# Performance work log

Measured on AMD Instinct MI355X. Metric: run time of the kernel, lower is better.

The kernel has to match this reference:

```python
import jax, jax.numpy as jnp
import numpy as np
from jax import lax

B, C, L = 4, 64, 4096
EPS = 1e-5  # BatchNorm1d default eps


def setup_inputs() -> dict:
    key = jax.random.key(0)
    ks = jax.random.split(key, 10)
    s_conv = 1.0 / np.sqrt(C * 3)
    s_1x1 = 1.0 / np.sqrt(C)
    return {
        "x": jax.random.normal(ks[0], (B, C, L), jnp.float32),
        "conv_w": jax.random.uniform(ks[1], (C, C, 3), jnp.float32, -s_conv, s_conv),
        "conv_b": jax.random.uniform(ks[2], (C,), jnp.float32, -s_conv, s_conv),
        "wq": jax.random.uniform(ks[3], (C, C), jnp.float32, -s_1x1, s_1x1),
        "bq": jax.random.uniform(ks[4], (C,), jnp.float32, -s_1x1, s_1x1),
        "wk": jax.random.uniform(ks[5], (C, C), jnp.float32, -s_1x1, s_1x1),
        "bk": jax.random.uniform(ks[6], (C,), jnp.float32, -s_1x1, s_1x1),
        "wv": jax.random.uniform(ks[7], (C, C), jnp.float32, -s_1x1, s_1x1),
        "bv": jax.random.uniform(ks[8], (C,), jnp.float32, -s_1x1, s_1x1),
        "gamma": jnp.ones((C,), jnp.float32),
        "beta": jnp.zeros((C,), jnp.float32),
    }


def reference(x, conv_w, conv_b, wq, bq, wk, bk, wv, bv, gamma, beta):
    residual = x
    h = jax.nn.elu(x)
    # circular padding for kernel-3 conv (padding=1, padding_mode='circular')
    hp = jnp.concatenate([h[:, :, -1:], h, h[:, :, :1]], axis=-1)  # [B,C,L+2]
    h = lax.conv_general_dilated(
        hp, conv_w, window_strides=(1,), padding="VALID",
        dimension_numbers=("NCH", "OIH", "NCH"),
    ) + conv_b[None, :, None]  # [B,C,L]
    # QKV 1x1 convs == per-position linear over channels
    q = jnp.einsum("oc,bcl->bol", wq, h) + bq[None, :, None]
    k = jnp.einsum("oc,bcl->bol", wk, h) + bk[None, :, None]
    v = jnp.einsum("oc,bcl->bol", wv, h) + bv[None, :, None]
    # SpatialGate: cm = q^T k [B,L,L]; out = v @ cm [B,C,L] (no softmax)
    cm = jnp.einsum("bcl,bcm->blm", q, k)
    g = jnp.einsum("bcl,blm->bcm", v, cm)
    y = g + residual
    # BatchNorm1d in training mode: per-channel stats over (B, L), biased var
    mean = jnp.mean(y, axis=(0, 2), keepdims=True)
    var = jnp.mean((y - mean) ** 2, axis=(0, 2), keepdims=True)
    out = gamma[None, :, None] * (y - mean) * lax.rsqrt(var + EPS) + beta[None, :, None]
    return out
```

## Files before the change

### kernel.cpp

```cpp
#include <hip/hip_runtime.h>
#include <math.h>

#define LDIM 4096
#define CDIM 64
#define NB 4
#define TL 64
#define NBLK (LDIM / TL)
#define NBLOCKS (NB * NBLK)
#define EPS 1e-5f
#define XS 68

#define K_OFF 0
#define Y_OFF (NB * CDIM * LDIM)
#define P_OFF (2 * NB * CDIM * LDIM)
#define M_OFF (P_OFF + NBLOCKS * CDIM * CDIM)
#define SP_OFF (M_OFF + NB * CDIM * CDIM)
#define S_OFF (SP_OFF + NBLOCKS * 2 * CDIM)

__device__ __forceinline__ float elu1(float t) { return t > 0.f ? t : expm1f(t); }

__global__ __launch_bounds__(1024, 4) void k_front(
    const float* __restrict__ x,
    const float* __restrict__ conv_w, const float* __restrict__ conv_b,
    const float* __restrict__ wq, const float* __restrict__ bq,
    const float* __restrict__ wk, const float* __restrict__ bk,
    const float* __restrict__ wv, const float* __restrict__ bv,
    float* __restrict__ k_ws, float* __restrict__ P_ws)
{
    __shared__ alignas(16) float xe[CDIM][XS];
    __shared__ alignas(16) float hs[CDIM][XS];
    __shared__ alignas(16) float qsT[TL][XS];
    __shared__ alignas(16) float vsT[TL][XS];

    const int b   = blockIdx.y;
    const int l0  = blockIdx.x * TL;
    const int tid = threadIdx.x;
    const int c   = tid >> 4;
    const int p0  = (tid & 15) << 2;

    const float* xb = x + (size_t)b * CDIM * LDIM;

    {
        float4 xv = *reinterpret_cast<const float4*>(xb + (size_t)c * LDIM + l0 + p0);
        xe[c][p0 + 1] = elu1(xv.x);
        xe[c][p0 + 2] = elu1(xv.y);
        xe[c][p0 + 3] = elu1(xv.z);
        xe[c][p0 + 4] = elu1(xv.w);
        if (tid < CDIM)
            xe[tid][0] = elu1(xb[(size_t)tid * LDIM + ((l0 - 1) & (LDIM - 1))]);
        else if (tid < 2 * CDIM)
            xe[tid - CDIM][TL + 1] =
                elu1(xb[(size_t)(tid - CDIM) * LDIM + ((l0 + TL) & (LDIM - 1))]);
    }
    __syncthreads();

    float hacc[4];
    {
        float cb = conv_b[c];
        hacc[0] = hacc[1] = hacc[2] = hacc[3] = cb;
    }
#pragma unroll 2
    for (int i4 = 0; i4 < 16; ++i4) {
        const float4* wrow = (const float4*)(conv_w + (size_t)c * 192 + i4 * 12);
        float4 f0 = wrow[0], f1 = wrow[1], f2 = wrow[2];
        float wx[4], wy[4], wz[4];
        wx[0] = f0.x; wy[0] = f0.y; wz[0] = f0.z;
        wx[1] = f0.w; wy[1] = f1.x; wz[1] = f1.y;
        wx[2] = f1.z; wy[2] = f1.w; wz[2] = f2.x;
        wx[3] = f2.y; wy[3] = f2.z; wz[3] = f2.w;
#pragma unroll
        for (int di = 0; di < 4; ++di) {
            const float* xr = &xe[i4 * 4 + di][p0];
            float4 a  = *reinterpret_cast<const float4*>(xr);
            float2 e2 = *reinterpret_cast<const float2*>(xr + 4);
            hacc[0] = fmaf(wx[di], a.x, fmaf(wy[di], a.y, fmaf(wz[di], a.z,  hacc[0])));
            hacc[1] = fmaf(wx[di], a.y, fmaf(wy[di], a.z, fmaf(wz[di], a.w,  hacc[1])));
            hacc[2] = fmaf(wx[di], a.z, fmaf(wy[di], a.w, fmaf(wz[di], e2.x, hacc[2])));
            hacc[3] = fmaf(wx[di], a.w, fmaf(wy[di], e2.x, fmaf(wz[di], e2.y, hacc[3])));
        }
    }
    *reinterpret_cast<float4*>(&hs[c][p0]) =
        make_float4(hacc[0], hacc[1], hacc[2], hacc[3]);
    __syncthreads();

    const float4* wq4 = (const float4*)wq;
    const float4* wk4 = (const float4*)wk;
    const float4* wv4 = (const float4*)wv;
    float qa[4], ka[4], va[4];
    {
        float t;
        t = bq[c]; qa[0] = qa[1] = qa[2] = qa[3] = t;
        t = bk[c]; ka[0] = ka[1] = ka[2] = ka[3] = t;
        t = bv[c]; va[0] = va[1] = va[2] = va[3] = t;
    }
#pragma unroll 2
    for (int i4 = 0; i4 < 16; ++i4) {
        float4 aq = wq4[c * 16 + i4];
        float4 ak = wk4[c * 16 + i4];
        float4 av = wv4[c * 16 + i4];
        float4 h0 = *reinterpret_cast<const float4*>(&hs[i4 * 4 + 0][p0]);
        float4 h1 = *reinterpret_cast<const float4*>(&hs[i4 * 4 + 1][p0]);
        float4 h2 = *reinterpret_cast<const float4*>(&hs[i4 * 4 + 2][p0]);
        float4 h3 = *reinterpret_cast<const float4*>(&hs[i4 * 4 + 3][p0]);
        qa[0] = fmaf(aq.x, h0.x, fmaf(aq.y, h1.x, fmaf(aq.z, h2.x, fmaf(aq.w, h3.x, qa[0]))));
        qa[1] = fmaf(aq.x, h0.y, fmaf(aq.y, h1.y, fmaf(aq.z, h2.y, fmaf(aq.w, h3.y, qa[1]))));
        qa[2] = fmaf(aq.x, h0.z, fmaf(aq.y, h1.z, fmaf(aq.z, h2.z, fmaf(aq.w, h3.z, qa[2]))));
        qa[3] = fmaf(aq.x, h0.w, fmaf(aq.y, h1.w, fmaf(aq.z, h2.w, fmaf(aq.w, h3.w, qa[3]))));
        ka[0] = fmaf(ak.x, h0.x, fmaf(ak.y, h1.x, fmaf(ak.z, h2.x, fmaf(ak.w, h3.x, ka[0]))));
        ka[1] = fmaf(ak.x, h0.y, fmaf(ak.y, h1.y, fmaf(ak.z, h2.y, fmaf(ak.w, h3.y, ka[1]))));
        ka[2] = fmaf(ak.x, h0.z, fmaf(ak.y, h1.z, fmaf(ak.z, h2.z, fmaf(ak.w, h3.z, ka[2]))));
        ka[3] = fmaf(ak.x, h0.w, fmaf(ak.y, h1.w, fmaf(ak.z, h2.w, fmaf(ak.w, h3.w, ka[3]))));
        va[0] = fmaf(av.x, h0.x, fmaf(av.y, h1.x, fmaf(av.z, h2.x, fmaf(av.w, h3.x, va[0]))));
        va[1] = fmaf(av.x, h0.y, fmaf(av.y, h1.y, fmaf(av.z, h2.y, fmaf(av.w, h3.y, va[1]))));
        va[2] = fmaf(av.x, h0.z, fmaf(av.y, h1.z, fmaf(av.z, h2.z, fmaf(av.w, h3.z, va[2]))));
        va[3] = fmaf(av.x, h0.w, fmaf(av.y, h1.w, fmaf(av.z, h2.w, fmaf(av.w, h3.w, va[3]))));
    }
    *reinterpret_cast<float4*>(k_ws + ((size_t)b * CDIM + c) * LDIM + l0 + p0) =
        make_float4(ka[0], ka[1], ka[2], ka[3]);
    qsT[p0 + 0][c] = qa[0]; qsT[p0 + 1][c] = qa[1];
    qsT[p0 + 2][c] = qa[2]; qsT[p0 + 3][c] = qa[3];
    vsT[p0 + 0][c] = va[0]; vsT[p0 + 1][c] = va[1];
    vsT[p0 + 2][c] = va[2]; vsT[p0 + 3][c] = va[3];
    __syncthreads();

    const int cv  = tid >> 4;
    const int cq0 = (tid & 15) * 4;
    float m0 = 0.f, m1 = 0.f, m2 = 0.f, m3 = 0.f;
    for (int l = 0; l < TL; ++l) {
        const float  vv = vsT[l][cv];
        const float4 qq = *reinterpret_cast<const float4*>(&qsT[l][cq0]);
        m0 = fmaf(vv, qq.x, m0);
        m1 = fmaf(vv, qq.y, m1);
        m2 = fmaf(vv, qq.z, m2);
        m3 = fmaf(vv, qq.w, m3);
    }
    float4* Pb = (float4*)(P_ws + ((size_t)b * NBLK + blockIdx.x) * CDIM * CDIM);
    Pb[cv * (CDIM / 4) + (cq0 >> 2)] = make_float4(m0, m1, m2, m3);
}

__global__ __launch_bounds__(256) void k_reduceM(
    const float* __restrict__ P_ws, float* __restrict__ M_ws)
{
    const int b  = blockIdx.x >> 2;
    const int e4 = (blockIdx.x & 3) * 256 + threadIdx.x;
    const float4* Pf4 = (const float4*)P_ws + (size_t)b * NBLK * (CDIM * CDIM / 4);
    float4 s0 = make_float4(0, 0, 0, 0), s1 = s0, s2 = s0, s3 = s0;
    for (int blk = 0; blk < NBLK; blk += 4) {
        float4 p0 = Pf4[(size_t)(blk + 0) * (CDIM * CDIM / 4) + e4];
        float4 p1 = Pf4[(size_t)(blk + 1) * (CDIM * CDIM / 4) + e4];
        float4 p2 = Pf4[(size_t)(blk + 2) * (CDIM * CDIM / 4) + e4];
        float4 p3 = Pf4[(size_t)(blk + 3) * (CDIM * CDIM / 4) + e4];
        s0.x += p0.x; s0.y += p0.y; s0.z += p0.z; s0.w += p0.w;
        s1.x += p1.x; s1.y += p1.y; s1.z += p1.z; s1.w += p1.w;
        s2.x += p2.x; s2.y += p2.y; s2.z += p2.z; s2.w += p2.w;
        s3.x += p3.x; s3.y += p3.y; s3.z += p3.z; s3.w += p3.w;
    }
    float4 s = make_float4((s0.x + s1.x) + (s2.x + s3.x),
                           (s0.y + s1.y) + (s2.y + s3.y),
                           (s0.z + s1.z) + (s2.z + s3.z),
                           (s0.w + s1.w) + (s2.w + s3.w));
    ((float4*)M_ws)[(size_t)b * (CDIM * CDIM / 4) + e4] = s;
}

__global__ __launch_bounds__(1024, 4) void k_spatial(
    const float* __restrict__ x, const float* __restrict__ k_ws,
    const float* __restrict__ M_ws, float* __restrict__ y_ws,
    float* __restrict__ spB)
{
    __shared__ alignas(16) float kl[CDIM][XS];
    __shared__ alignas(16) float Ms[CDIM][XS];
    const int b   = blockIdx.y;
    const int l0  = blockIdx.x * TL;
    const int tid = threadIdx.x;
    const int c   = tid >> 4;
    const int p0  = (tid & 15) << 2;

    *reinterpret_cast<float4*>(&Ms[c][p0]) =
        ((const float4*)M_ws)[(size_t)b * (CDIM * CDIM / 4) + tid];
    *reinterpret_cast<float4*>(&kl[c][p0]) =
        *reinterpret_cast<const float4*>(k_ws + ((size_t)b * CDIM + c) * LDIM + l0 + p0);
    __syncthreads();

    float4 acc = *reinterpret_cast<const float4*>(
        x + ((size_t)b * CDIM + c) * LDIM + l0 + p0);
#pragma unroll 2
    for (int i4 = 0; i4 < 16; ++i4) {
        float4 mv = *reinterpret_cast<const float4*>(&Ms[c][i4 * 4]);
        float4 k0 = *reinterpret_cast<const float4*>(&kl[i4 * 4 + 0][p0]);
        float4 k1 = *reinterpret_cast<const float4*>(&kl[i4 * 4 + 1][p0]);
        float4 k2 = *reinterpret_cast<const float4*>(&kl[i4 * 4 + 2][p0]);
        float4 k3 = *reinterpret_cast<const float4*>(&kl[i4 * 4 + 3][p0]);
        acc.x = fmaf(mv.x, k0.x, fmaf(mv.y, k1.x, fmaf(mv.z, k2.x, fmaf(mv.w, k3.x, acc.x))));
        acc.y = fmaf(mv.x, k0.y, fmaf(mv.y, k1.y, fmaf(mv.z, k2.y, fmaf(mv.w, k3.y, acc.y))));
        acc.z = fmaf(mv.x, k0.z, fmaf(mv.y, k1.z, fmaf(mv.z, k2.z, fmaf(mv.w, k3.z, acc.z))));
        acc.w = fmaf(mv.x, k0.w, fmaf(mv.y, k1.w, fmaf(mv.z, k2.w, fmaf(mv.w, k3.w, acc.w))));
    }
    *reinterpret_cast<float4*>(y_ws + ((size_t)b * CDIM + c) * LDIM + l0 + p0) = acc;

    const int blk = blockIdx.y * NBLK + blockIdx.x;
    float s  = (acc.x + acc.y) + (acc.z + acc.w);
    float s2 = fmaf(acc.x, acc.x, fmaf(acc.y, acc.y,
               fmaf(acc.z, acc.z, acc.w * acc.w)));
    for (int off = 8; off; off >>= 1) {
        s  += __shfl_down(s, off);
        s2 += __shfl_down(s2, off);
    }
    if ((tid & 15) == 0) {
        spB[(size_t)blk * (2 * CDIM) + c] = s;
        spB[(size_t)blk * (2 * CDIM) + CDIM + c] = s2;
    }
}

__global__ __launch_bounds__(512) void k_reduceS(
    const float* __restrict__ spB, float* __restrict__ sums)
{
    __shared__ float red[4][128];
    const int t = threadIdx.x & 127;
    const int q = threadIdx.x >> 7;
    float s0 = 0.f, s1 = 0.f, s2 = 0.f, s3 = 0.f;
    const int r0 = q * 64;
    for (int r = r0; r < r0 + 64; r += 4) {
        s0 += spB[(r + 0) * (2 * CDIM) + t];
        s1 += spB[(r + 1) * (2 * CDIM) + t];
        s2 += spB[(r + 2) * (2 * CDIM) + t];
        s3 += spB[(r + 3) * (2 * CDIM) + t];
    }
    red[q][t] = (s0 + s1) + (s2 + s3);
    __syncthreads();
    if (threadIdx.x < 128)
        sums[t] = (red[0][t] + red[1][t]) + (red[2][t] + red[3][t]);
}

__global__ __launch_bounds__(256) void k_norm(
    const float* __restrict__ y_ws, const float* __restrict__ sums,
    const float* __restrict__ gamma, const float* __restrict__ beta,
    float* __restrict__ out)
{
    const int idx = blockIdx.x * 256 + threadIdx.x;
    const int c   = (idx >> 10) & (CDIM - 1);
    const float inv = 1.f / (float)(NB * LDIM);
    float s    = sums[c];
    float s2   = sums[CDIM + c];
    float mean = s * inv;
    float var  = fmaf(-mean, mean, s2 * inv);
    float rstd = 1.f / sqrtf(var + EPS);
    float g    = gamma[c] * rstd;
    float bb   = fmaf(-mean, g, beta[c]);

    float4 v = ((const float4*)y_ws)[idx];
    float4 o;
    o.x = fmaf(v.x, g, bb);
    o.y = fmaf(v.y, g, bb);
    o.z = fmaf(v.z, g, bb);
    o.w = fmaf(v.w, g, bb);
    ((float4*)out)[idx] = o;
}

extern "C" void kernel_launch(void* const* d_in, const int* in_sizes, int n_in,
                              void* d_out, int out_size, void* d_ws, size_t ws_size,
                              hipStream_t stream)
{
    const float* x      = (const float*)d_in[0];
    const float* conv_w = (const float*)d_in[1];
    const float* conv_b = (const float*)d_in[2];
    const float* wq     = (const float*)d_in[3];
    const float* bq     = (const float*)d_in[4];
    const float* wk     = (const float*)d_in[5];
    const float* bk     = (const float*)d_in[6];
    const float* wv     = (const float*)d_in[7];
    const float* bv     = (const float*)d_in[8];
    const float* gamma  = (const float*)d_in[9];
    const float* beta   = (const float*)d_in[10];

    float* ws   = (float*)d_ws;
    float* k_ws = ws + K_OFF;
    float* y_ws = ws + Y_OFF;
    float* P_ws = ws + P_OFF;
    float* M_ws = ws + M_OFF;
    float* spB  = ws + SP_OFF;
    float* sums = ws + S_OFF;

    dim3 grid(NBLK, NB);
    k_front<<<grid, 1024, 0, stream>>>(x, conv_w, conv_b, wq, bq, wk, bk,
                                       wv, bv, k_ws, P_ws);
    k_reduceM<<<16, 256, 0, stream>>>(P_ws, M_ws);
    k_spatial<<<grid, 1024, 0, stream>>>(x, k_ws, M_ws, y_ws, spB);
    k_reduceS<<<1, 512, 0, stream>>>(spB, sums);

    const int n4 = NB * CDIM * LDIM / 4;
    k_norm<<<n4 / 256, 256, 0, stream>>>(y_ws, sums, gamma, beta, (float*)d_out);
}
```

Measured before the change: 122.8 us.

## Halve front-kernel tile width and fold stats reduction into normalize kernel

The front kernel now processes 32 positions per block with 512 threads, doubling the grid to 512 blocks, which spreads work over more CUs. Each thread computes 8 outputs of the partial v·qT product, and the partial buffer and the M reduction loop are resized to match. The separate single-block stats reduction kernel is removed. Every normalize block now redundantly reduces the per-block channel sums into shared memory before applying BatchNorm, saving one launch at the cost of duplicated reads of the small partials buffer.

```diff
diff --git a/kernel.cpp b/kernel.cpp
--- a/kernel.cpp
+++ b/kernel.cpp
@@ -6,20 +6,22 @@
 #define NB 4
 #define TL 64
 #define NBLK (LDIM / TL)
+#define TLF 32
+#define NBLKF (LDIM / TLF)
 #define NBLOCKS (NB * NBLK)
 #define EPS 1e-5f
 #define XS 68
+#define XSF 36
 
 #define K_OFF 0
 #define Y_OFF (NB * CDIM * LDIM)
 #define P_OFF (2 * NB * CDIM * LDIM)
-#define M_OFF (P_OFF + NBLOCKS * CDIM * CDIM)
+#define M_OFF (P_OFF + NB * NBLKF * CDIM * CDIM)
 #define SP_OFF (M_OFF + NB * CDIM * CDIM)
-#define S_OFF (SP_OFF + NBLOCKS * 2 * CDIM)
 
 __device__ __forceinline__ float elu1(float t) { return t > 0.f ? t : expm1f(t); }
 
-__global__ __launch_bounds__(1024, 4) void k_front(
+__global__ __launch_bounds__(512, 4) void k_front(
     const float* __restrict__ x,
     const float* __restrict__ conv_w, const float* __restrict__ conv_b,
     const float* __restrict__ wq, const float* __restrict__ bq,
@@ -27,16 +29,16 @@
     const float* __restrict__ wv, const float* __restrict__ bv,
     float* __restrict__ k_ws, float* __restrict__ P_ws)
 {
-    __shared__ alignas(16) float xe[CDIM][XS];
-    __shared__ alignas(16) float hs[CDIM][XS];
-    __shared__ alignas(16) float qsT[TL][XS];
-    __shared__ alignas(16) float vsT[TL][XS];
+    __shared__ alignas(16) float xe[CDIM][XSF];
+    __shared__ alignas(16) float hs[CDIM][XSF];
+    __shared__ alignas(16) float qsT[TLF][XS];
+    __shared__ alignas(16) float vsT[TLF][XS];
 
     const int b   = blockIdx.y;
-    const int l0  = blockIdx.x * TL;
+    const int l0  = blockIdx.x * TLF;
     const int tid = threadIdx.x;
-    const int c   = tid >> 4;
-    const int p0  = (tid & 15) << 2;
+    const int c   = tid >> 3;
+    const int p0  = (tid & 7) << 2;
 
     const float* xb = x + (size_t)b * CDIM * LDIM;
 
@@ -49,8 +51,8 @@
         if (tid < CDIM)
             xe[tid][0] = elu1(xb[(size_t)tid * LDIM + ((l0 - 1) & (LDIM - 1))]);
         else if (tid < 2 * CDIM)
-            xe[tid - CDIM][TL + 1] =
-                elu1(xb[(size_t)(tid - CDIM) * LDIM + ((l0 + TL) & (LDIM - 1))]);
+            xe[tid - CDIM][TLF + 1] =
+                elu1(xb[(size_t)(tid - CDIM) * LDIM + ((l0 + TLF) & (LDIM - 1))]);
     }
     __syncthreads();
 
@@ -123,19 +125,21 @@
     vsT[p0 + 2][c] = va[2]; vsT[p0 + 3][c] = va[3];
     __syncthreads();
 
-    const int cv  = tid >> 4;
-    const int cq0 = (tid & 15) * 4;
-    float m0 = 0.f, m1 = 0.f, m2 = 0.f, m3 = 0.f;
-    for (int l = 0; l < TL; ++l) {
+    const int cv  = tid >> 3;
+    const int cq0 = (tid & 7) * 8;
+    float m[8] = {0.f, 0.f, 0.f, 0.f, 0.f, 0.f, 0.f, 0.f};
+    for (int l = 0; l < TLF; ++l) {
         const float  vv = vsT[l][cv];
-        const float4 qq = *reinterpret_cast<const float4*>(&qsT[l][cq0]);
-        m0 = fmaf(vv, qq.x, m0);
-        m1 = fmaf(vv, qq.y, m1);
-        m2 = fmaf(vv, qq.z, m2);
-        m3 = fmaf(vv, qq.w, m3);
-    }
-    float4* Pb = (float4*)(P_ws + ((size_t)b * NBLK + blockIdx.x) * CDIM * CDIM);
-    Pb[cv * (CDIM / 4) + (cq0 >> 2)] = make_float4(m0, m1, m2, m3);
+        const float4 qA = *reinterpret_cast<const float4*>(&qsT[l][cq0]);
+        const float4 qB = *reinterpret_cast<const float4*>(&qsT[l][cq0 + 4]);
+        m[0] = fmaf(vv, qA.x, m[0]); m[1] = fmaf(vv, qA.y, m[1]);
+        m[2] = fmaf(vv, qA.z, m[2]); m[3] = fmaf(vv, qA.w, m[3]);
+        m[4] = fmaf(vv, qB.x, m[4]); m[5] = fmaf(vv, qB.y, m[5]);
+        m[6] = fmaf(vv, qB.z, m[6]); m[7] = fmaf(vv, qB.w, m[7]);
+    }
+    float4* Pb = (float4*)(P_ws + ((size_t)b * NBLKF + blockIdx.x) * CDIM * CDIM);
+    Pb[cv * (CDIM / 4) + (cq0 >> 2) + 0] = make_float4(m[0], m[1], m[2], m[3]);
+    Pb[cv * (CDIM / 4) + (cq0 >> 2) + 1] = make_float4(m[4], m[5], m[6], m[7]);
 }
 
 __global__ __launch_bounds__(256) void k_reduceM(
@@ -143,9 +147,9 @@
 {
     const int b  = blockIdx.x >> 2;
     const int e4 = (blockIdx.x & 3) * 256 + threadIdx.x;
-    const float4* Pf4 = (const float4*)P_ws + (size_t)b * NBLK * (CDIM * CDIM / 4);
+    const float4* Pf4 = (const float4*)P_ws + (size_t)b * NBLKF * (CDIM * CDIM / 4);
     float4 s0 = make_float4(0, 0, 0, 0), s1 = s0, s2 = s0, s3 = s0;
-    for (int blk = 0; blk < NBLK; blk += 4) {
+    for (int blk = 0; blk < NBLKF; blk += 4) {
         float4 p0 = Pf4[(size_t)(blk + 0) * (CDIM * CDIM / 4) + e4];
         float4 p1 = Pf4[(size_t)(blk + 1) * (CDIM * CDIM / 4) + e4];
         float4 p2 = Pf4[(size_t)(blk + 2) * (CDIM * CDIM / 4) + e4];
@@ -211,38 +215,37 @@
     }
 }
 
-__global__ __launch_bounds__(512) void k_reduceS(
-    const float* __restrict__ spB, float* __restrict__ sums)
-{
-    __shared__ float red[4][128];
-    const int t = threadIdx.x & 127;
-    const int q = threadIdx.x >> 7;
-    float s0 = 0.f, s1 = 0.f, s2 = 0.f, s3 = 0.f;
-    const int r0 = q * 64;
-    for (int r = r0; r < r0 + 64; r += 4) {
-        s0 += spB[(r + 0) * (2 * CDIM) + t];
-        s1 += spB[(r + 1) * (2 * CDIM) + t];
-        s2 += spB[(r + 2) * (2 * CDIM) + t];
-        s3 += spB[(r + 3) * (2 * CDIM) + t];
-    }
-    red[q][t] = (s0 + s1) + (s2 + s3);
-    __syncthreads();
-    if (threadIdx.x < 128)
-        sums[t] = (red[0][t] + red[1][t]) + (red[2][t] + red[3][t]);
-}
-
-__global__ __launch_bounds__(256) void k_norm(
-    const float* __restrict__ y_ws, const float* __restrict__ sums,
+__global__ __launch_bounds__(1024) void k_normS(
+    const float* __restrict__ y_ws, const float* __restrict__ spB,
     const float* __restrict__ gamma, const float* __restrict__ beta,
     float* __restrict__ out)
 {
-    const int idx = blockIdx.x * 256 + threadIdx.x;
+    __shared__ float red[8][128];
+    __shared__ float sums2[2 * CDIM];
+    const int tid = threadIdx.x;
+
+    {
+        const int t = tid & 127;
+        const int g = tid >> 7;
+        float s0 = 0.f, s1 = 0.f;
+        const int r0 = g * 32;
+        for (int r = r0; r < r0 + 32; r += 2) {
+            s0 += spB[(size_t)(r + 0) * (2 * CDIM) + t];
+            s1 += spB[(size_t)(r + 1) * (2 * CDIM) + t];
+        }
+        red[g][t] = s0 + s1;
+    }
+    __syncthreads();
+    if (tid < 128)
+        sums2[tid] = ((red[0][tid] + red[1][tid]) + (red[2][tid] + red[3][tid]))
+                   + ((red[4][tid] + red[5][tid]) + (red[6][tid] + red[7][tid]));
+    __syncthreads();
+
+    const int idx = blockIdx.x * 1024 + tid;
     const int c   = (idx >> 10) & (CDIM - 1);
     const float inv = 1.f / (float)(NB * LDIM);
-    float s    = sums[c];
-    float s2   = sums[CDIM + c];
-    float mean = s * inv;
-    float var  = fmaf(-mean, mean, s2 * inv);
+    float mean = sums2[c] * inv;
+    float var  = fmaf(-mean, mean, sums2[CDIM + c] * inv);
     float rstd = 1.f / sqrtf(var + EPS);
     float g    = gamma[c] * rstd;
     float bb   = fmaf(-mean, g, beta[c]);
@@ -278,15 +281,13 @@
     float* P_ws = ws + P_OFF;
     float* M_ws = ws + M_OFF;
     float* spB  = ws + SP_OFF;
-    float* sums = ws + S_OFF;
-
-    dim3 grid(NBLK, NB);
-    k_front<<<grid, 1024, 0, stream>>>(x, conv_w, conv_b, wq, bq, wk, bk,
+
+    dim3 gridF(NBLKF, NB);
+    dim3 gridS(NBLK, NB);
+    k_front<<<gridF, 512, 0, stream>>>(x, conv_w, conv_b, wq, bq, wk, bk,
                                        wv, bv, k_ws, P_ws);
     k_reduceM<<<16, 256, 0, stream>>>(P_ws, M_ws);
-    k_spatial<<<grid, 1024, 0, stream>>>(x, k_ws, M_ws, y_ws, spB);
-    k_reduceS<<<1, 512, 0, stream>>>(spB, sums);
-
-    const int n4 = NB * CDIM * LDIM / 4;
-    k_norm<<<n4 / 256, 256, 0, stream>>>(y_ws, sums, gamma, beta, (float*)d_out);
-}
+    k_spatial<<<gridS, 1024, 0, stream>>>(x, k_ws, M_ws, y_ws, spB);
+    k_normS<<<NB * CDIM * LDIM / 4096, 1024, 0, stream>>>(y_ws, spB, gamma, beta,
+                                                          (float*)d_out);
+}
```

Result: no change. 123.1 us (+0.3%).

## Fuse partial-sum reductions into spatial and normalization kernels

Applied to the files above, without the earlier changes.

Removes the separate reduceM and reduceS kernels. Each spatial block now sums the per-tile P partials for its batch directly, and each normalization block reduces the per-block channel statistics itself. The aim is to cut kernel launches and their serialization gaps. In exchange, every block repeats the full reduction, which greatly multiplies global/L2 read traffic for the P partials.

```diff
diff --git a/kernel.cpp b/kernel.cpp
--- a/kernel.cpp
+++ b/kernel.cpp
@@ -13,9 +13,7 @@
 #define K_OFF 0
 #define Y_OFF (NB * CDIM * LDIM)
 #define P_OFF (2 * NB * CDIM * LDIM)
-#define M_OFF (P_OFF + NBLOCKS * CDIM * CDIM)
-#define SP_OFF (M_OFF + NB * CDIM * CDIM)
-#define S_OFF (SP_OFF + NBLOCKS * 2 * CDIM)
+#define SP_OFF (P_OFF + NB * NBLK * CDIM * CDIM)
 
 __device__ __forceinline__ float elu1(float t) { return t > 0.f ? t : expm1f(t); }
 
@@ -138,33 +136,9 @@
     Pb[cv * (CDIM / 4) + (cq0 >> 2)] = make_float4(m0, m1, m2, m3);
 }
 
-__global__ __launch_bounds__(256) void k_reduceM(
-    const float* __restrict__ P_ws, float* __restrict__ M_ws)
-{
-    const int b  = blockIdx.x >> 2;
-    const int e4 = (blockIdx.x & 3) * 256 + threadIdx.x;
-    const float4* Pf4 = (const float4*)P_ws + (size_t)b * NBLK * (CDIM * CDIM / 4);
-    float4 s0 = make_float4(0, 0, 0, 0), s1 = s0, s2 = s0, s3 = s0;
-    for (int blk = 0; blk < NBLK; blk += 4) {
-        float4 p0 = Pf4[(size_t)(blk + 0) * (CDIM * CDIM / 4) + e4];
-        float4 p1 = Pf4[(size_t)(blk + 1) * (CDIM * CDIM / 4) + e4];
-        float4 p2 = Pf4[(size_t)(blk + 2) * (CDIM * CDIM / 4) + e4];
-        float4 p3 = Pf4[(size_t)(blk + 3) * (CDIM * CDIM / 4) + e4];
-        s0.x += p0.x; s0.y += p0.y; s0.z += p0.z; s0.w += p0.w;
-        s1.x += p1.x; s1.y += p1.y; s1.z += p1.z; s1.w += p1.w;
-        s2.x += p2.x; s2.y += p2.y; s2.z += p2.z; s2.w += p2.w;
-        s3.x += p3.x; s3.y += p3.y; s3.z += p3.z; s3.w += p3.w;
-    }
-    float4 s = make_float4((s0.x + s1.x) + (s2.x + s3.x),
-                           (s0.y + s1.y) + (s2.y + s3.y),
-                           (s0.z + s1.z) + (s2.z + s3.z),
-                           (s0.w + s1.w) + (s2.w + s3.w));
-    ((float4*)M_ws)[(size_t)b * (CDIM * CDIM / 4) + e4] = s;
-}
-
 __global__ __launch_bounds__(1024, 4) void k_spatial(
     const float* __restrict__ x, const float* __restrict__ k_ws,
-    const float* __restrict__ M_ws, float* __restrict__ y_ws,
+    const float* __restrict__ P_ws, float* __restrict__ y_ws,
     float* __restrict__ spB)
 {
     __shared__ alignas(16) float kl[CDIM][XS];
@@ -175,8 +149,25 @@
     const int c   = tid >> 4;
     const int p0  = (tid & 15) << 2;
 
-    *reinterpret_cast<float4*>(&Ms[c][p0]) =
-        ((const float4*)M_ws)[(size_t)b * (CDIM * CDIM / 4) + tid];
+    {
+        const float4* Pf4 = (const float4*)P_ws + (size_t)b * NBLK * (CDIM * CDIM / 4);
+        float4 s0 = make_float4(0, 0, 0, 0), s1 = s0, s2 = s0, s3 = s0;
+        for (int blk = 0; blk < NBLK; blk += 4) {
+            float4 p0v = Pf4[(size_t)(blk + 0) * (CDIM * CDIM / 4) + tid];
+            float4 p1v = Pf4[(size_t)(blk + 1) * (CDIM * CDIM / 4) + tid];
+            float4 p2v = Pf4[(size_t)(blk + 2) * (CDIM * CDIM / 4) + tid];
+            float4 p3v = Pf4[(size_t)(blk + 3) * (CDIM * CDIM / 4) + tid];
+            s0.x += p0v.x; s0.y += p0v.y; s0.z += p0v.z; s0.w += p0v.w;
+            s1.x += p1v.x; s1.y += p1v.y; s1.z += p1v.z; s1.w += p1v.w;
+            s2.x += p2v.x; s2.y += p2v.y; s2.z += p2v.z; s2.w += p2v.w;
+            s3.x += p3v.x; s3.y += p3v.y; s3.z += p3v.z; s3.w += p3v.w;
+        }
+        *reinterpret_cast<float4*>(&Ms[c][p0]) =
+            make_float4((s0.x + s1.x) + (s2.x + s3.x),
+                        (s0.y + s1.y) + (s2.y + s3.y),
+                        (s0.z + s1.z) + (s2.z + s3.z),
+                        (s0.w + s1.w) + (s2.w + s3.w));
+    }
     *reinterpret_cast<float4*>(&kl[c][p0]) =
         *reinterpret_cast<const float4*>(k_ws + ((size_t)b * CDIM + c) * LDIM + l0 + p0);
     __syncthreads();
@@ -211,38 +202,37 @@
     }
 }
 
-__global__ __launch_bounds__(512) void k_reduceS(
-    const float* __restrict__ spB, float* __restrict__ sums)
-{
-    __shared__ float red[4][128];
-    const int t = threadIdx.x & 127;
-    const int q = threadIdx.x >> 7;
-    float s0 = 0.f, s1 = 0.f, s2 = 0.f, s3 = 0.f;
-    const int r0 = q * 64;
-    for (int r = r0; r < r0 + 64; r += 4) {
-        s0 += spB[(r + 0) * (2 * CDIM) + t];
-        s1 += spB[(r + 1) * (2 * CDIM) + t];
-        s2 += spB[(r + 2) * (2 * CDIM) + t];
-        s3 += spB[(r + 3) * (2 * CDIM) + t];
-    }
-    red[q][t] = (s0 + s1) + (s2 + s3);
-    __syncthreads();
-    if (threadIdx.x < 128)
-        sums[t] = (red[0][t] + red[1][t]) + (red[2][t] + red[3][t]);
-}
-
-__global__ __launch_bounds__(256) void k_norm(
-    const float* __restrict__ y_ws, const float* __restrict__ sums,
+__global__ __launch_bounds__(1024) void k_normS(
+    const float* __restrict__ y_ws, const float* __restrict__ spB,
     const float* __restrict__ gamma, const float* __restrict__ beta,
     float* __restrict__ out)
 {
-    const int idx = blockIdx.x * 256 + threadIdx.x;
+    __shared__ float red[8][128];
+    __shared__ float sums2[2 * CDIM];
+    const int tid = threadIdx.x;
+
+    {
+        const int t = tid & 127;
+        const int g = tid >> 7;
+        float s0 = 0.f, s1 = 0.f;
+        const int r0 = g * 32;
+        for (int r = r0; r < r0 + 32; r += 2) {
+            s0 += spB[(size_t)(r + 0) * (2 * CDIM) + t];
+            s1 += spB[(size_t)(r + 1) * (2 * CDIM) + t];
+        }
+        red[g][t] = s0 + s1;
+    }
+    __syncthreads();
+    if (tid < 128)
+        sums2[tid] = ((red[0][tid] + red[1][tid]) + (red[2][tid] + red[3][tid]))
+                   + ((red[4][tid] + red[5][tid]) + (red[6][tid] + red[7][tid]));
+    __syncthreads();
+
+    const int idx = blockIdx.x * 1024 + tid;
     const int c   = (idx >> 10) & (CDIM - 1);
     const float inv = 1.f / (float)(NB * LDIM);
-    float s    = sums[c];
-    float s2   = sums[CDIM + c];
-    float mean = s * inv;
-    float var  = fmaf(-mean, mean, s2 * inv);
+    float mean = sums2[c] * inv;
+    float var  = fmaf(-mean, mean, sums2[CDIM + c] * inv);
     float rstd = 1.f / sqrtf(var + EPS);
     float g    = gamma[c] * rstd;
     float bb   = fmaf(-mean, g, beta[c]);
@@ -276,17 +266,12 @@
     float* k_ws = ws + K_OFF;
     float* y_ws = ws + Y_OFF;
     float* P_ws = ws + P_OFF;
-    float* M_ws = ws + M_OFF;
     float* spB  = ws + SP_OFF;
-    float* sums = ws + S_OFF;
 
     dim3 grid(NBLK, NB);
     k_front<<<grid, 1024, 0, stream>>>(x, conv_w, conv_b, wq, bq, wk, bk,
                                        wv, bv, k_ws, P_ws);
-    k_reduceM<<<16, 256, 0, stream>>>(P_ws, M_ws);
-    k_spatial<<<grid, 1024, 0, stream>>>(x, k_ws, M_ws, y_ws, spB);
-    k_reduceS<<<1, 512, 0, stream>>>(spB, sums);
-
-    const int n4 = NB * CDIM * LDIM / 4;
-    k_norm<<<n4 / 256, 256, 0, stream>>>(y_ws, sums, gamma, beta, (float*)d_out);
-}
+    k_spatial<<<grid, 1024, 0, stream>>>(x, k_ws, P_ws, y_ws, spB);
+    k_normS<<<NB * CDIM * LDIM / 4096, 1024, 0, stream>>>(y_ws, spB, gamma, beta,
+                                                          (float*)d_out);
+}
```

After: 120.9 us. No clear change (-1.5%).
